# Optimization experiments

Hardware: AMD Instinct MI355X
Metric: run time of the kernel (lower is better)

The kernel has to match this reference:

```python
import jax, jax.numpy as jnp
import numpy as np

F_IN = 512
N_STAGES = 6
BATCH = 16384


def entmax15_1d(v):
    # Exact entmax with alpha=1.5 on a 1D vector (Peters et al. 2019).
    x = (v - jnp.max(v)) * 0.5
    xs = jnp.sort(x)[::-1]                      # descending
    rho = jnp.arange(1, xs.shape[0] + 1, dtype=xs.dtype)
    mean = jnp.cumsum(xs) / rho
    mean_sq = jnp.cumsum(xs * xs) / rho
    ss = rho * (mean_sq - mean * mean)
    delta = jnp.clip((1.0 - ss) / rho, 0.0, None)
    tau = mean - jnp.sqrt(delta)
    support_size = jnp.sum(tau <= xs)
    tau_star = tau[support_size - 1]
    return jnp.square(jnp.clip(x - tau_star, 0.0, None))


def setup_inputs() -> dict:
    key = jax.random.key(0)
    ks = jax.random.split(key, 7)
    F2 = 2 * F_IN
    lim_in = 1.0 / np.sqrt(F2)   # torch Linear default init bound (fan_in = 2F)
    x = jax.random.normal(ks[0], (BATCH, F_IN), dtype=jnp.float32)
    masks = jax.random.uniform(ks[1], (N_STAGES, F_IN), dtype=jnp.float32)  # Beta-sampled in torch; uniform(0,1) is in-range
    Win_w = jax.random.uniform(ks[2], (N_STAGES, F2, F2), minval=-lim_in, maxval=lim_in, dtype=jnp.float32)
    Win_b = jax.random.uniform(ks[3], (N_STAGES, F2), minval=-lim_in, maxval=lim_in, dtype=jnp.float32)
    Wout_w = jax.random.uniform(ks[4], (N_STAGES, F_IN, F2), minval=-lim_in, maxval=lim_in, dtype=jnp.float32)
    Wout_b = jax.random.uniform(ks[5], (N_STAGES, F_IN), minval=-lim_in, maxval=lim_in, dtype=jnp.float32)
    return {"x": x, "masks": masks, "Win_w": Win_w, "Win_b": Win_b,
            "Wout_w": Wout_w, "Wout_b": Wout_b}


def reference(x, masks, Win_w, Win_b, Wout_w, Wout_b):
    F = x.shape[-1]
    h = x
    for d in range(N_STAGES):
        feature = entmax15_1d(masks[d]) * x                      # [B, F]
        h_in = jnp.concatenate([feature, h], axis=-1) @ Win_w[d].T + Win_b[d]  # [B, 2F]
        z = jax.nn.sigmoid(h_in[:, :F])
        r = jax.nn.sigmoid(h_in[:, F:])
        h_out = jnp.tanh(jnp.concatenate([r * h, x], axis=-1) @ Wout_w[d].T + Wout_b[d])
        h = (1.0 - z) * h + z * h_out                            # dropout p=0 -> identity
    return h
```

## Files before the change

### kernel.cpp

```cpp
#include <hip/hip_runtime.h>
#include <stdint.h>
#include <math.h>

typedef unsigned short u16;
typedef short s16x8 __attribute__((ext_vector_type(8)));
typedef float f32x4 __attribute__((ext_vector_type(4)));
typedef u16 u16x4 __attribute__((ext_vector_type(4)));

#define FDIM 512
#define F2 1024
#define BATCH 16384
#define NST 6
#define KDIM 1024
#define NT 32

__device__ __forceinline__ u16 f2bf(float f) {
  uint32_t u = __float_as_uint(f);
  u += 0x7FFFu + ((u >> 16) & 1u);
  return (u16)(u >> 16);
}
__device__ __forceinline__ float bf2f(u16 b) {
  return __uint_as_float((uint32_t)b << 16);
}

#define LOG2E 1.44269504f
__device__ __forceinline__ float fast_sigmoid(float v) {
  float e = __builtin_amdgcn_exp2f(-v * LOG2E);
  return __builtin_amdgcn_rcpf(1.0f + e);
}
__device__ __forceinline__ float fast_tanh(float v) {
  float e = __builtin_amdgcn_exp2f(v * (2.0f * LOG2E));
  return 1.0f - 2.0f * __builtin_amdgcn_rcpf(1.0f + e);
}

__device__ __forceinline__ void ld_lds16(u16* lds, const u16* g) {
  __builtin_amdgcn_global_load_lds(
      (const __attribute__((address_space(1))) uint32_t*)g,
      (__attribute__((address_space(3))) uint32_t*)lds, 16, 0, 0);
}

__global__ __launch_bounds__(512) void entmax_kernel(const float* __restrict__ masks,
                                                     float* __restrict__ fm) {
  __shared__ float sx[FDIM];
  __shared__ float ssort[FDIM];
  __shared__ float stau[FDIM];
  __shared__ float2 sc[2][FDIM];
  const int d = blockIdx.x;
  const int j = threadIdx.x;
  float v = masks[d * FDIM + j];

  stau[j] = v;
  __syncthreads();
  for (int s = 256; s > 0; s >>= 1) {
    if (j < s) stau[j] = fmaxf(stau[j], stau[j + s]);
    __syncthreads();
  }
  float mx = stau[0];
  __syncthreads();

  float xx = (v - mx) * 0.5f;
  sx[j] = xx;
  __syncthreads();

  int r = 0;
  const float4* sx4 = (const float4*)sx;
#pragma unroll 4
  for (int i4 = 0; i4 < FDIM / 4; i4++) {
    float4 q = sx4[i4];
    int i = i4 << 2;
    r += (q.x > xx) || (q.x == xx && (i + 0) < j);
    r += (q.y > xx) || (q.y == xx && (i + 1) < j);
    r += (q.z > xx) || (q.z == xx && (i + 2) < j);
    r += (q.w > xx) || (q.w == xx && (i + 3) < j);
  }
  ssort[r] = xx;
  __syncthreads();
  float xs = ssort[j];

  sc[0][j] = make_float2(xs, xs * xs);
  __syncthreads();
  int pp = 0;
  for (int off = 1; off < FDIM; off <<= 1) {
    float2 t = sc[pp][j];
    if (j >= off) {
      float2 u = sc[pp][j - off];
      t.x += u.x;
      t.y += u.y;
    }
    sc[pp ^ 1][j] = t;
    __syncthreads();
    pp ^= 1;
  }
  float2 cs = sc[pp][j];

  float rho = (float)(j + 1);
  float mean = cs.x / rho;
  float msq = cs.y / rho;
  float ss = rho * (msq - mean * mean);
  float delta = (1.f - ss) / rho;
  if (delta < 0.f) delta = 0.f;
  float tau = mean - sqrtf(delta);
  stau[j] = tau;
  int cnt = __syncthreads_count(tau <= xs);
  float tstar = stau[cnt - 1];
  float c = fmaxf(xx - tstar, 0.f);
  fm[d * FDIM + j] = c * c;
}

__global__ __launch_bounds__(256) void cvt_w1_kernel(const float* __restrict__ src,
                                                     const float* __restrict__ fm,
                                                     u16* __restrict__ dst) {
  int t = blockIdx.x * 256 + threadIdx.x;
  int k = (t & 255) << 2;
  int dn = t >> 8;
  int d = dn >> 10;
  float4 v = *(const float4*)(src + (size_t)t * 4);
  if (k < FDIM) {
    float4 s = *(const float4*)(fm + (size_t)d * FDIM + k);
    v.x *= s.x; v.y *= s.y; v.z *= s.z; v.w *= s.w;
  }
  u16x4 o = {f2bf(v.x), f2bf(v.y), f2bf(v.z), f2bf(v.w)};
  *(u16x4*)(dst + (size_t)t * 4) = o;
}

__global__ __launch_bounds__(256) void cvt_kernel(const float* __restrict__ src,
                                                  u16* __restrict__ dst, int n4) {
  int t = blockIdx.x * blockDim.x + threadIdx.x;
  if (t >= n4) return;
  float4 v = *(const float4*)(src + (size_t)t * 4);
  u16x4 o = {f2bf(v.x), f2bf(v.y), f2bf(v.z), f2bf(v.w)};
  *(u16x4*)(dst + (size_t)t * 4) = o;
}

__global__ __launch_bounds__(256) void fill_xbf_kernel(const float* __restrict__ x,
                                                       u16* __restrict__ A1,
                                                       u16* __restrict__ A2) {
  int t = blockIdx.x * blockDim.x + threadIdx.x;
  int m = t >> 7;
  int c = (t & 127) << 2;
  float4 xv = *(const float4*)(x + (size_t)m * FDIM + c);
  u16x4 o = {f2bf(xv.x), f2bf(xv.y), f2bf(xv.z), f2bf(xv.w)};
  *(u16x4*)(A1 + (size_t)m * F2 + c) = o;
  *(u16x4*)(A1 + (size_t)m * F2 + FDIM + c) = o;
  *(u16x4*)(A2 + (size_t)m * F2 + FDIM + c) = o;
}

__device__ __forceinline__ void gemm_core8(const u16* __restrict__ Ag,
                                           const u16* __restrict__ Bg,
                                           int m0, int n0, u16* smem,
                                           f32x4 acc[8][4]) {
  const int tid = threadIdx.x;
  const int lane = tid & 63;
  const int wid = tid >> 6;
  const int wm = wid >> 2;
  const int wn = wid & 3;

  const int rs = tid >> 2;
  const int colsw = ((tid & 3) ^ ((rs >> 1) & 3)) << 3;
  const u16* gA0 = Ag + (size_t)(m0 + rs) * KDIM + colsw;
  const u16* gA1 = gA0 + (size_t)128 * KDIM;
  const u16* gB0 = Bg + (size_t)(n0 + rs) * KDIM + colsw;
  const u16* gB1 = gB0 + (size_t)128 * KDIM;
  const int lds_u = tid * 8;

  const int fcs = ((lane >> 4) ^ ((lane >> 1) & 3)) << 3;
  const int aoff = (wm * 128 + (lane & 15)) * 32 + fcs;
  const int boff = (wn * 64 + (lane & 15)) * 32 + fcs;

#pragma unroll
  for (int i = 0; i < 8; i++)
#pragma unroll
    for (int j = 0; j < 4; j++) acc[i][j] = (f32x4){0.f, 0.f, 0.f, 0.f};

#pragma unroll
  for (int kt = 0; kt < 3; kt++) {
    u16* rb = smem + kt * 16384;
    ld_lds16(rb + lds_u, gA0 + kt * 32);
    ld_lds16(rb + 4096 + lds_u, gA1 + kt * 32);
    ld_lds16(rb + 8192 + lds_u, gB0 + kt * 32);
    ld_lds16(rb + 12288 + lds_u, gB1 + kt * 32);
  }
  asm volatile("s_waitcnt vmcnt(8)" ::: "memory");
  __builtin_amdgcn_s_barrier();
  __builtin_amdgcn_sched_barrier(0);

  for (int t = 0; t < NT; t++) {
    const u16* rb = smem + (t & 3) * 16384;
    u16* sb = smem + ((t + 3) & 3) * 16384;
    if (t + 3 < NT) {
      ld_lds16(sb + lds_u, gA0 + (t + 3) * 32);
      ld_lds16(sb + 4096 + lds_u, gA1 + (t + 3) * 32);
      ld_lds16(sb + 8192 + lds_u, gB0 + (t + 3) * 32);
      ld_lds16(sb + 12288 + lds_u, gB1 + (t + 3) * 32);
    }
    s16x8 af[8], bfr[4];
#pragma unroll
    for (int f = 0; f < 8; f++)
      af[f] = *(const s16x8*)(rb + aoff + f * 512);
#pragma unroll
    for (int g = 0; g < 4; g++)
      bfr[g] = *(const s16x8*)(rb + 8192 + boff + g * 512);
    if (t < NT - 3) {
      asm volatile("s_waitcnt vmcnt(8)" ::: "memory");
    } else if (t == NT - 3) {
      asm volatile("s_waitcnt vmcnt(4)" ::: "memory");
    } else if (t == NT - 2) {
      asm volatile("s_waitcnt vmcnt(0)" ::: "memory");
    }
    __builtin_amdgcn_s_setprio(1);
#pragma unroll
    for (int f = 0; f < 8; f++)
#pragma unroll
      for (int g = 0; g < 4; g++)
        acc[f][g] = __builtin_amdgcn_mfma_f32_16x16x32_bf16(af[f], bfr[g], acc[f][g], 0, 0, 0);
    __builtin_amdgcn_s_setprio(0);
    __builtin_amdgcn_sched_barrier(0);
    __builtin_amdgcn_s_barrier();
    __builtin_amdgcn_sched_barrier(0);
  }
}

__device__ __forceinline__ void gemm_core4(const u16* __restrict__ Ag,
                                           const u16* __restrict__ Bg,
                                           int m0, int n0, u16* smem,
                                           f32x4 acc[4][4]) {
  const int tid = threadIdx.x;
  const int lane = tid & 63;
  const int wid = tid >> 6;
  const int wm = wid >> 2;
  const int wn = wid & 3;

  const int rs = tid >> 2;
  const int colsw = ((tid & 3) ^ ((rs >> 1) & 3)) << 3;
  const u16* gA0 = Ag + (size_t)(m0 + rs) * KDIM + colsw;
  const u16* gB0 = Bg + (size_t)(n0 + rs) * KDIM + colsw;
  const u16* gB1 = gB0 + (size_t)128 * KDIM;
  const int lds_u = tid * 8;

  const int fcs = ((lane >> 4) ^ ((lane >> 1) & 3)) << 3;
  const int aoff = (wm * 64 + (lane & 15)) * 32 + fcs;
  const int boff = (wn * 64 + (lane & 15)) * 32 + fcs;

#pragma unroll
  for (int i = 0; i < 4; i++)
#pragma unroll
    for (int j = 0; j < 4; j++) acc[i][j] = (f32x4){0.f, 0.f, 0.f, 0.f};

#pragma unroll
  for (int kt = 0; kt < 3; kt++) {
    u16* rb = smem + kt * 12288;
    ld_lds16(rb + lds_u, gA0 + kt * 32);
    ld_lds16(rb + 4096 + lds_u, gB0 + kt * 32);
    ld_lds16(rb + 8192 + lds_u, gB1 + kt * 32);
  }
  asm volatile("s_waitcnt vmcnt(6)" ::: "memory");
  __builtin_amdgcn_s_barrier();
  __builtin_amdgcn_sched_barrier(0);

  for (int t = 0; t < NT; t++) {
    const u16* rb = smem + (t & 3) * 12288;
    u16* sb = smem + ((t + 3) & 3) * 12288;
    if (t + 3 < NT) {
      ld_lds16(sb + lds_u, gA0 + (t + 3) * 32);
      ld_lds16(sb + 4096 + lds_u, gB0 + (t + 3) * 32);
      ld_lds16(sb + 8192 + lds_u, gB1 + (t + 3) * 32);
    }
    s16x8 af[4], bfr[4];
#pragma unroll
    for (int f = 0; f < 4; f++)
      af[f] = *(const s16x8*)(rb + aoff + f * 512);
#pragma unroll
    for (int g = 0; g < 4; g++)
      bfr[g] = *(const s16x8*)(rb + 4096 + boff + g * 512);
    if (t < NT - 3) {
      asm volatile("s_waitcnt vmcnt(6)" ::: "memory");
    } else if (t == NT - 3) {
      asm volatile("s_waitcnt vmcnt(3)" ::: "memory");
    } else if (t == NT - 2) {
      asm volatile("s_waitcnt vmcnt(0)" ::: "memory");
    }
    __builtin_amdgcn_s_setprio(1);
#pragma unroll
    for (int f = 0; f < 4; f++)
#pragma unroll
      for (int g = 0; g < 4; g++)
        acc[f][g] = __builtin_amdgcn_mfma_f32_16x16x32_bf16(af[f], bfr[g], acc[f][g], 0, 0, 0);
    __builtin_amdgcn_s_setprio(0);
    __builtin_amdgcn_sched_barrier(0);
    __builtin_amdgcn_s_barrier();
    __builtin_amdgcn_sched_barrier(0);
  }
}

__global__ __launch_bounds__(512, 2) void gemm1_kernel(const u16* __restrict__ A1,
                                                       const u16* __restrict__ W1,
                                                       const float* __restrict__ b1,
                                                       _Float16* __restrict__ zbuf,
                                                       u16* __restrict__ A2) {
  __shared__ u16 smem[65536];
  const int bx = blockIdx.x;
  const int wg = (bx & 7) * 32 + (bx >> 3);
  const int m0 = (wg >> 2) << 8;
  const int n0 = (wg & 3) << 8;
  f32x4 acc[8][4];
  gemm_core8(A1, W1, m0, n0, smem, acc);

  const int lane = threadIdx.x & 63;
  const int wid = threadIdx.x >> 6;
  const int wm = wid >> 2;
  const int wn = wid & 3;
  const int fcol = lane & 15;
  const int frow = (lane >> 4) << 2;

  if (n0 < FDIM) {
#pragma unroll
    for (int f = 0; f < 8; f++)
#pragma unroll
      for (int g = 0; g < 4; g++)
#pragma unroll
        for (int r = 0; r < 4; r++) {
          int gm = m0 + wm * 128 + f * 16 + frow + r;
          int gn = n0 + wn * 64 + g * 16 + fcol;
          float v = acc[f][g][r] + b1[gn];
          zbuf[(size_t)gm * FDIM + gn] = (_Float16)fast_sigmoid(v);
        }
  } else {
#pragma unroll
    for (int f = 0; f < 8; f++)
#pragma unroll
      for (int g = 0; g < 4; g++)
#pragma unroll
        for (int r = 0; r < 4; r++) {
          int gm = m0 + wm * 128 + f * 16 + frow + r;
          int gn = n0 + wn * 64 + g * 16 + fcol;
          float v = acc[f][g][r] + b1[gn];
          float s = fast_sigmoid(v);
          int c = gn - FDIM;
          float h = bf2f(A1[(size_t)gm * F2 + FDIM + c]);
          A2[(size_t)gm * F2 + c] = f2bf(s * h);
        }
  }
}

__global__ __launch_bounds__(512, 2) void gemm2_kernel(const u16* __restrict__ A2,
                                                       const u16* __restrict__ W2,
                                                       const float* __restrict__ b2,
                                                       const _Float16* __restrict__ zbuf,
                                                       u16* __restrict__ A1,
                                                       float* __restrict__ out,
                                                       int last) {
  __shared__ u16 smem[49152];
  const int bx = blockIdx.x;
  const int wg = (bx & 7) * 32 + (bx >> 3);
  const int m0 = (wg >> 1) << 7;
  const int n0 = (wg & 1) << 8;
  f32x4 acc[4][4];
  gemm_core4(A2, W2, m0, n0, smem, acc);

  const int lane = threadIdx.x & 63;
  const int wid = threadIdx.x >> 6;
  const int wm = wid >> 2;
  const int wn = wid & 3;
  const int fcol = lane & 15;
  const int frow = (lane >> 4) << 2;

#pragma unroll
  for (int f = 0; f < 4; f++)
#pragma unroll
    for (int g = 0; g < 4; g++)
#pragma unroll
      for (int r = 0; r < 4; r++) {
        int gm = m0 + wm * 64 + f * 16 + frow + r;
        int gn = n0 + wn * 64 + g * 16 + fcol;
        float v = acc[f][g][r] + b2[gn];
        float ho = fast_tanh(v);
        size_t idx = (size_t)gm * FDIM + gn;
        float z = (float)zbuf[idx];
        float hv = bf2f(A1[(size_t)gm * F2 + FDIM + gn]);
        float hn = (1.0f - z) * hv + z * ho;
        if (last)
          out[idx] = hn;
        else
          A1[(size_t)gm * F2 + FDIM + gn] = f2bf(hn);
      }
}

extern "C" void kernel_launch(void* const* d_in, const int* in_sizes, int n_in,
                              void* d_out, int out_size, void* d_ws, size_t ws_size,
                              hipStream_t stream) {
  (void)in_sizes; (void)n_in; (void)out_size; (void)ws_size;
  const float* x = (const float*)d_in[0];
  const float* masks = (const float*)d_in[1];
  const float* W1f = (const float*)d_in[2];
  const float* b1 = (const float*)d_in[3];
  const float* W2f = (const float*)d_in[4];
  const float* b2 = (const float*)d_in[5];

  char* ws = (char*)d_ws;
  float* fm = (float*)ws;       ws += (size_t)NST * FDIM * 4;
  u16* W1b = (u16*)ws;          ws += (size_t)NST * F2 * F2 * 2;
  u16* W2b = (u16*)ws;          ws += (size_t)NST * FDIM * F2 * 2;
  u16* A1 = (u16*)ws;           ws += (size_t)BATCH * F2 * 2;
  u16* A2 = (u16*)ws;           ws += (size_t)BATCH * F2 * 2;
  _Float16* zbuf = (_Float16*)ws; ws += (size_t)BATCH * FDIM * 2;
  float* out = (float*)d_out;

  entmax_kernel<<<NST, 512, 0, stream>>>(masks, fm);
  cvt_w1_kernel<<<NST * F2 * F2 / 4 / 256, 256, 0, stream>>>(W1f, fm, W1b);
  {
    int n4 = NST * FDIM * F2 / 4;
    cvt_kernel<<<(n4 + 255) / 256, 256, 0, stream>>>(W2f, W2b, n4);
  }
  fill_xbf_kernel<<<BATCH * 128 / 256, 256, 0, stream>>>(x, A1, A2);

  for (int d = 0; d < NST; d++) {
    gemm1_kernel<<<(BATCH / 256) * (F2 / 256), 512, 0, stream>>>(
        A1, W1b + (size_t)d * F2 * F2, b1 + d * F2, zbuf, A2);
    gemm2_kernel<<<(BATCH / 128) * (FDIM / 256), 512, 0, stream>>>(
        A2, W2b + (size_t)d * FDIM * F2, b2 + d * FDIM, zbuf,
        A1, out, d == NST - 1);
  }
}
```

Baseline: 497.6 us.

## Use unified 128x128 GEMM tile with 256 threads and 3-stage LDS pipeline

Both GEMMs now share one 128x128-tile core run by 4 waves, with a 2x2 wave layout and 64x64 per wave. The ring drops from 4 to 3 LDS buffers with prefetch depth 2, and occupancy rises to 3 blocks per CU. This launches more, smaller blocks for better load balance and cuts LDS use. The cost is lower arithmetic intensity per block, more global traffic for operands, and less latency hiding from the shallower prefetch.

```diff
diff --git a/kernel.cpp b/kernel.cpp
--- a/kernel.cpp
+++ b/kernel.cpp
@@ -145,71 +145,73 @@
   *(u16x4*)(A2 + (size_t)m * F2 + FDIM + c) = o;
 }
 
-__device__ __forceinline__ void gemm_core8(const u16* __restrict__ Ag,
-                                           const u16* __restrict__ Bg,
-                                           int m0, int n0, u16* smem,
-                                           f32x4 acc[8][4]) {
+__device__ __forceinline__ void gemm_core128(const u16* __restrict__ Ag,
+                                             const u16* __restrict__ Bg,
+                                             int m0, int n0, u16* smem,
+                                             f32x4 acc[4][4]) {
   const int tid = threadIdx.x;
   const int lane = tid & 63;
   const int wid = tid >> 6;
-  const int wm = wid >> 2;
-  const int wn = wid & 3;
+  const int wm = wid >> 1;
+  const int wn = wid & 1;
 
   const int rs = tid >> 2;
   const int colsw = ((tid & 3) ^ ((rs >> 1) & 3)) << 3;
   const u16* gA0 = Ag + (size_t)(m0 + rs) * KDIM + colsw;
-  const u16* gA1 = gA0 + (size_t)128 * KDIM;
+  const u16* gA1 = gA0 + (size_t)64 * KDIM;
   const u16* gB0 = Bg + (size_t)(n0 + rs) * KDIM + colsw;
-  const u16* gB1 = gB0 + (size_t)128 * KDIM;
+  const u16* gB1 = gB0 + (size_t)64 * KDIM;
   const int lds_u = tid * 8;
 
   const int fcs = ((lane >> 4) ^ ((lane >> 1) & 3)) << 3;
-  const int aoff = (wm * 128 + (lane & 15)) * 32 + fcs;
-  const int boff = (wn * 64 + (lane & 15)) * 32 + fcs;
-
-#pragma unroll
-  for (int i = 0; i < 8; i++)
+  const int aoff = (wm * 64 + (lane & 15)) * 32 + fcs;
+  const int boff = 4096 + (wn * 64 + (lane & 15)) * 32 + fcs;
+
+#pragma unroll
+  for (int i = 0; i < 4; i++)
 #pragma unroll
     for (int j = 0; j < 4; j++) acc[i][j] = (f32x4){0.f, 0.f, 0.f, 0.f};
 
 #pragma unroll
-  for (int kt = 0; kt < 3; kt++) {
-    u16* rb = smem + kt * 16384;
+  for (int kt = 0; kt < 2; kt++) {
+    u16* rb = smem + kt * 8192;
     ld_lds16(rb + lds_u, gA0 + kt * 32);
-    ld_lds16(rb + 4096 + lds_u, gA1 + kt * 32);
-    ld_lds16(rb + 8192 + lds_u, gB0 + kt * 32);
-    ld_lds16(rb + 12288 + lds_u, gB1 + kt * 32);
-  }
-  asm volatile("s_waitcnt vmcnt(8)" ::: "memory");
+    ld_lds16(rb + 2048 + lds_u, gA1 + kt * 32);
+    ld_lds16(rb + 4096 + lds_u, gB0 + kt * 32);
+    ld_lds16(rb + 6144 + lds_u, gB1 + kt * 32);
+  }
+  asm volatile("s_waitcnt vmcnt(4)" ::: "memory");
   __builtin_amdgcn_s_barrier();
   __builtin_amdgcn_sched_barrier(0);
 
+  int ci = 0;
   for (int t = 0; t < NT; t++) {
-    const u16* rb = smem + (t & 3) * 16384;
-    u16* sb = smem + ((t + 3) & 3) * 16384;
-    if (t + 3 < NT) {
-      ld_lds16(sb + lds_u, gA0 + (t + 3) * 32);
-      ld_lds16(sb + 4096 + lds_u, gA1 + (t + 3) * 32);
-      ld_lds16(sb + 8192 + lds_u, gB0 + (t + 3) * 32);
-      ld_lds16(sb + 12288 + lds_u, gB1 + (t + 3) * 32);
+    const u16* rb = smem + ci * 8192;
+    int si = ci + 2;
+    if (si >= 3) si -= 3;
+    u16* sb = smem + si * 8192;
+    if (t + 2 < NT) {
+      const int k0 = (t + 2) * 32;
+      ld_lds16(sb + lds_u, gA0 + k0);
+      ld_lds16(sb + 2048 + lds_u, gA1 + k0);
+      ld_lds16(sb + 4096 + lds_u, gB0 + k0);
+      ld_lds16(sb + 6144 + lds_u, gB1 + k0);
     }
-    s16x8 af[8], bfr[4];
-#pragma unroll
-    for (int f = 0; f < 8; f++)
+    s16x8 af[4], bfr[4];
+#pragma unroll
+    for (int f = 0; f < 4; f++)
       af[f] = *(const s16x8*)(rb + aoff + f * 512);
 #pragma unroll
     for (int g = 0; g < 4; g++)
-      bfr[g] = *(const s16x8*)(rb + 8192 + boff + g * 512);
-    if (t < NT - 3) {
-      asm volatile("s_waitcnt vmcnt(8)" ::: "memory");
-    } else if (t == NT - 3) {
+      bfr[g] = *(const s16x8*)(rb + boff + g * 512);
+    if (t < NT - 2) {
       asm volatile("s_waitcnt vmcnt(4)" ::: "memory");
     } else if (t == NT - 2) {
       asm volatile("s_waitcnt vmcnt(0)" ::: "memory");
     }
     __builtin_amdgcn_s_setprio(1);
 #pragma unroll
-    for (int f = 0; f < 8; f++)
+    for (int f = 0; f < 4; f++)
 #pragma unroll
       for (int g = 0; g < 4; g++)
         acc[f][g] = __builtin_amdgcn_mfma_f32_16x16x32_bf16(af[f], bfr[g], acc[f][g], 0, 0, 0);
@@ -217,121 +219,51 @@
     __builtin_amdgcn_sched_barrier(0);
     __builtin_amdgcn_s_barrier();
     __builtin_amdgcn_sched_barrier(0);
-  }
-}
-
-__device__ __forceinline__ void gemm_core4(const u16* __restrict__ Ag,
-                                           const u16* __restrict__ Bg,
-                                           int m0, int n0, u16* smem,
-                                           f32x4 acc[4][4]) {
-  const int tid = threadIdx.x;
-  const int lane = tid & 63;
-  const int wid = tid >> 6;
-  const int wm = wid >> 2;
-  const int wn = wid & 3;
-
-  const int rs = tid >> 2;
-  const int colsw = ((tid & 3) ^ ((rs >> 1) & 3)) << 3;
-  const u16* gA0 = Ag + (size_t)(m0 + rs) * KDIM + colsw;
-  const u16* gB0 = Bg + (size_t)(n0 + rs) * KDIM + colsw;
-  const u16* gB1 = gB0 + (size_t)128 * KDIM;
-  const int lds_u = tid * 8;
-
-  const int fcs = ((lane >> 4) ^ ((lane >> 1) & 3)) << 3;
-  const int aoff = (wm * 64 + (lane & 15)) * 32 + fcs;
-  const int boff = (wn * 64 + (lane & 15)) * 32 + fcs;
-
-#pragma unroll
-  for (int i = 0; i < 4; i++)
-#pragma unroll
-    for (int j = 0; j < 4; j++) acc[i][j] = (f32x4){0.f, 0.f, 0.f, 0.f};
-
-#pragma unroll
-  for (int kt = 0; kt < 3; kt++) {
-    u16* rb = smem + kt * 12288;
-    ld_lds16(rb + lds_u, gA0 + kt * 32);
-    ld_lds16(rb + 4096 + lds_u, gB0 + kt * 32);
-    ld_lds16(rb + 8192 + lds_u, gB1 + kt * 32);
-  }
-  asm volatile("s_waitcnt vmcnt(6)" ::: "memory");
-  __builtin_amdgcn_s_barrier();
-  __builtin_amdgcn_sched_barrier(0);
-
-  for (int t = 0; t < NT; t++) {
-    const u16* rb = smem + (t & 3) * 12288;
-    u16* sb = smem + ((t + 3) & 3) * 12288;
-    if (t + 3 < NT) {
-      ld_lds16(sb + lds_u, gA0 + (t + 3) * 32);
-      ld_lds16(sb + 4096 + lds_u, gB0 + (t + 3) * 32);
-      ld_lds16(sb + 8192 + lds_u, gB1 + (t + 3) * 32);
-    }
-    s16x8 af[4], bfr[4];
-#pragma unroll
-    for (int f = 0; f < 4; f++)
-      af[f] = *(const s16x8*)(rb + aoff + f * 512);
-#pragma unroll
-    for (int g = 0; g < 4; g++)
-      bfr[g] = *(const s16x8*)(rb + 4096 + boff + g * 512);
-    if (t < NT - 3) {
-      asm volatile("s_waitcnt vmcnt(6)" ::: "memory");
-    } else if (t == NT - 3) {
-      asm volatile("s_waitcnt vmcnt(3)" ::: "memory");
-    } else if (t == NT - 2) {
-      asm volatile("s_waitcnt vmcnt(0)" ::: "memory");
-    }
-    __builtin_amdgcn_s_setprio(1);
-#pragma unroll
-    for (int f = 0; f < 4; f++)
-#pragma unroll
-      for (int g = 0; g < 4; g++)
-        acc[f][g] = __builtin_amdgcn_mfma_f32_16x16x32_bf16(af[f], bfr[g], acc[f][g], 0, 0, 0);
-    __builtin_amdgcn_s_setprio(0);
-    __builtin_amdgcn_sched_barrier(0);
-    __builtin_amdgcn_s_barrier();
-    __builtin_amdgcn_sched_barrier(0);
-  }
-}
-
-__global__ __launch_bounds__(512, 2) void gemm1_kernel(const u16* __restrict__ A1,
+    ci = ci + 1;
+    if (ci == 3) ci = 0;
+  }
+}
+
+__global__ __launch_bounds__(256, 3) void gemm1_kernel(const u16* __restrict__ A1,
                                                        const u16* __restrict__ W1,
                                                        const float* __restrict__ b1,
                                                        _Float16* __restrict__ zbuf,
                                                        u16* __restrict__ A2) {
-  __shared__ u16 smem[65536];
+  __shared__ u16 smem[24576];
   const int bx = blockIdx.x;
-  const int wg = (bx & 7) * 32 + (bx >> 3);
-  const int m0 = (wg >> 2) << 8;
-  const int n0 = (wg & 3) << 8;
-  f32x4 acc[8][4];
-  gemm_core8(A1, W1, m0, n0, smem, acc);
+  const int wg = (bx & 7) * 128 + (bx >> 3);
+  const int m0 = (wg >> 3) << 7;
+  const int n0 = (wg & 7) << 7;
+  f32x4 acc[4][4];
+  gemm_core128(A1, W1, m0, n0, smem, acc);
 
   const int lane = threadIdx.x & 63;
   const int wid = threadIdx.x >> 6;
-  const int wm = wid >> 2;
-  const int wn = wid & 3;
+  const int wm = wid >> 1;
+  const int wn = wid & 1;
   const int fcol = lane & 15;
   const int frow = (lane >> 4) << 2;
 
   if (n0 < FDIM) {
 #pragma unroll
-    for (int f = 0; f < 8; f++)
+    for (int f = 0; f < 4; f++)
 #pragma unroll
       for (int g = 0; g < 4; g++)
 #pragma unroll
         for (int r = 0; r < 4; r++) {
-          int gm = m0 + wm * 128 + f * 16 + frow + r;
+          int gm = m0 + wm * 64 + f * 16 + frow + r;
           int gn = n0 + wn * 64 + g * 16 + fcol;
           float v = acc[f][g][r] + b1[gn];
           zbuf[(size_t)gm * FDIM + gn] = (_Float16)fast_sigmoid(v);
         }
   } else {
 #pragma unroll
-    for (int f = 0; f < 8; f++)
+    for (int f = 0; f < 4; f++)
 #pragma unroll
       for (int g = 0; g < 4; g++)
 #pragma unroll
         for (int r = 0; r < 4; r++) {
-          int gm = m0 + wm * 128 + f * 16 + frow + r;
+          int gm = m0 + wm * 64 + f * 16 + frow + r;
           int gn = n0 + wn * 64 + g * 16 + fcol;
           float v = acc[f][g][r] + b1[gn];
           float s = fast_sigmoid(v);
@@ -342,25 +274,25 @@
   }
 }
 
-__global__ __launch_bounds__(512, 2) void gemm2_kernel(const u16* __restrict__ A2,
+__global__ __launch_bounds__(256, 3) void gemm2_kernel(const u16* __restrict__ A2,
                                                        const u16* __restrict__ W2,
                                                        const float* __restrict__ b2,
                                                        const _Float16* __restrict__ zbuf,
                                                        u16* __restrict__ A1,
                                                        float* __restrict__ out,
                                                        int last) {
-  __shared__ u16 smem[49152];
+  __shared__ u16 smem[24576];
   const int bx = blockIdx.x;
-  const int wg = (bx & 7) * 32 + (bx >> 3);
-  const int m0 = (wg >> 1) << 7;
-  const int n0 = (wg & 1) << 8;
+  const int wg = (bx & 7) * 64 + (bx >> 3);
+  const int m0 = (wg >> 2) << 7;
+  const int n0 = (wg & 3) << 7;
   f32x4 acc[4][4];
-  gemm_core4(A2, W2, m0, n0, smem, acc);
+  gemm_core128(A2, W2, m0, n0, smem, acc);
 
   const int lane = threadIdx.x & 63;
   const int wid = threadIdx.x >> 6;
-  const int wm = wid >> 2;
-  const int wn = wid & 3;
+  const int wm = wid >> 1;
+  const int wn = wid & 1;
   const int fcol = lane & 15;
   const int frow = (lane >> 4) << 2;
 
@@ -414,9 +346,9 @@
   fill_xbf_kernel<<<BATCH * 128 / 256, 256, 0, stream>>>(x, A1, A2);
 
   for (int d = 0; d < NST; d++) {
-    gemm1_kernel<<<(BATCH / 256) * (F2 / 256), 512, 0, stream>>>(
+    gemm1_kernel<<<(BATCH / 128) * (F2 / 128), 256, 0, stream>>>(
         A1, W1b + (size_t)d * F2 * F2, b1 + d * F2, zbuf, A2);
-    gemm2_kernel<<<(BATCH / 128) * (FDIM / 256), 512, 0, stream>>>(
+    gemm2_kernel<<<(BATCH / 128) * (FDIM / 128), 256, 0, stream>>>(
         A2, W2b + (size_t)d * FDIM * F2, b2 + d * FDIM, zbuf,
         A1, out, d == NST - 1);
   }
```

Measured after the change: 561.7 us. 12.9% more time.
